# Kernel optimization log

Hardware: AMD Instinct MI355X
Metric: run time of the kernel (lower is better)

## Reference

```python
import jax, jax.numpy as jnp
import numpy as np
from jax import lax

B, S, T = 512, 64, 32
E, H = 512, 1024
VIN, VOUT = 128, 128


def gru_cell(x, h, W_ih, W_hh, b_ih, b_hh):
    # PyTorch GRU cell: gates ordered (r, z, n)
    gi = x @ W_ih.T + b_ih           # [B, 3*Hh]
    gh = h @ W_hh.T + b_hh           # [B, 3*Hh]
    i_r, i_z, i_n = jnp.split(gi, 3, axis=-1)
    h_r, h_z, h_n = jnp.split(gh, 3, axis=-1)
    r = jax.nn.sigmoid(i_r + h_r)
    z = jax.nn.sigmoid(i_z + h_z)
    n = jnp.tanh(i_n + r * h_n)
    return (1.0 - z) * n + z * h


def setup_inputs() -> dict:
    key = jax.random.key(0)
    ks = jax.random.split(key, 18)
    g = lambda k, shp: (jax.random.normal(k, shp, jnp.float32) * 0.05)
    return {
        "src": jax.random.randint(ks[0], (B, S), 0, VIN),
        "tgt": jax.random.randint(ks[1], (B, T), 0, VOUT),
        "enc_emb": g(ks[2], (VIN, E)),
        "dec_emb": g(ks[3], (VOUT, E)),
        "W_ih_f": g(ks[4], (3 * H, E)), "W_hh_f": g(ks[5], (3 * H, H)),
        "b_ih_f": g(ks[6], (3 * H,)), "b_hh_f": g(ks[7], (3 * H,)),
        "W_ih_b": g(ks[8], (3 * H, E)), "W_hh_b": g(ks[9], (3 * H, H)),
        "b_ih_b": g(ks[10], (3 * H,)), "b_hh_b": g(ks[11], (3 * H,)),
        "W_ih_d": g(ks[12], (3 * 2 * H, E)), "W_hh_d": g(ks[13], (3 * 2 * H, 2 * H)),
        "b_ih_d": g(ks[14], (3 * 2 * H,)), "b_hh_d": g(ks[15], (3 * 2 * H,)),
        "W_fc": g(ks[16], (VOUT, 2 * H)), "b_fc": g(ks[17], (VOUT,)),
    }


def reference(src, tgt, enc_emb, dec_emb,
              W_ih_f, W_hh_f, b_ih_f, b_hh_f,
              W_ih_b, W_hh_b, b_ih_b, b_hh_b,
              W_ih_d, W_hh_d, b_ih_d, b_hh_d,
              W_fc, b_fc):
    batch = src.shape[0]
    x = enc_emb[src]                         # [B, S, E]
    x_t = jnp.swapaxes(x, 0, 1)              # [S, B, E]

    def enc_scan(xs, W_ih, W_hh, b_ih, b_hh):
        h0 = jnp.zeros((batch, H), dtype=xs.dtype)
        def step(h, xt):
            h2 = gru_cell(xt, h, W_ih, W_hh, b_ih, b_hh)
            return h2, None
        hT, _ = lax.scan(step, h0, xs)
        return hT                             # final hidden [B, H]

    h_fwd = enc_scan(x_t, W_ih_f, W_hh_f, b_ih_f, b_hh_f)
    h_bwd = enc_scan(x_t[::-1], W_ih_b, W_hh_b, b_ih_b, b_hh_b)
    h = jnp.concatenate([h_fwd, h_bwd], axis=-1)   # [B, 2H] = torch.cat((h[-2], h[-1]), 1)

    tok0 = tgt[:, 0]                          # <sos> tokens

    def dec_step(carry, _):
        hh, tok = carry
        xt = dec_emb[tok]                     # [B, E]
        hh = gru_cell(xt, hh, W_ih_d, W_hh_d, b_ih_d, b_hh_d)
        logits = hh @ W_fc.T + b_fc           # [B, VOUT]
        nxt = jnp.argmax(logits, axis=-1)     # greedy feedback (teacher_forcing_ratio=0)
        return (hh, nxt), logits

    (_, _), logits = lax.scan(dec_step, (h, tok0), None, length=tgt.shape[1] - 1)
    return jnp.swapaxes(logits, 0, 1)         # [B, T-1, VOUT]
```

## Files before the change

### kernel.cpp

```cpp
#include <hip/hip_runtime.h>
#include <math.h>

#define B 512
#define S 64
#define T 32
#define E 512
#define H 1024
#define VOUTD 128
#define H2 (2*H)
#define H3 (3*H)
#define H6 (6*H)

#define LDR 40

typedef unsigned short ushortT;
typedef unsigned int uintT;
typedef __attribute__((ext_vector_type(8))) short short8;
typedef __attribute__((ext_vector_type(4))) float floatx4;

__device__ __forceinline__ float sigmoidf_(float x) { return 1.0f / (1.0f + expf(-x)); }

__global__ __launch_bounds__(256) void split_bf16(
    const float4* __restrict__ x, uint2* __restrict__ hi, uint2* __restrict__ lo, int n4)
{
    int i = blockIdx.x * 256 + threadIdx.x;
    if (i >= n4) return;
    float4 v = x[i];
    uintT ux = __float_as_uint(v.x), uy = __float_as_uint(v.y);
    uintT uz = __float_as_uint(v.z), uw = __float_as_uint(v.w);
    uintT lx = __float_as_uint(v.x - __uint_as_float(ux & 0xFFFF0000u)) >> 16;
    uintT ly = __float_as_uint(v.y - __uint_as_float(uy & 0xFFFF0000u)) >> 16;
    uintT lz = __float_as_uint(v.z - __uint_as_float(uz & 0xFFFF0000u)) >> 16;
    uintT lw = __float_as_uint(v.w - __uint_as_float(uw & 0xFFFF0000u)) >> 16;
    hi[i] = make_uint2((ux >> 16) | (uy & 0xFFFF0000u), (uz >> 16) | (uw & 0xFFFF0000u));
    lo[i] = make_uint2(lx | (ly << 16), lz | (lw << 16));
}

__global__ __launch_bounds__(256) void zero16(uint4* __restrict__ p, int n)
{
    int i = blockIdx.x * 256 + threadIdx.x;
    if (i < n) p[i] = make_uint4(0u, 0u, 0u, 0u);
}

__global__ __launch_bounds__(256) void fused_step_enc(
    const ushortT* __restrict__ Ahi, const ushortT* __restrict__ Alo,
    const ushortT* __restrict__ Whi_f, const ushortT* __restrict__ Wlo_f,
    const ushortT* __restrict__ Whi_b, const ushortT* __restrict__ Wlo_b,
    const float* __restrict__ giTabF, const float* __restrict__ giTabB,
    const int* __restrict__ src, int s,
    const float* __restrict__ bhF, const float* __restrict__ bhB,
    float* __restrict__ h,
    ushortT* __restrict__ hiOut, ushortT* __restrict__ loOut)
{
    __shared__ ushortT sAh[2][64 * LDR], sAl[2][64 * LDR];
    __shared__ ushortT sBh[2][96 * LDR], sBl[2][96 * LDR];
    __shared__ int sTok[64];

    const int t    = threadIdx.x;
    const int lane = t & 63;
    const int w    = t >> 6;

    const int bid = blockIdx.x;
    const int xcd = bid & 7;
    const int q   = bid >> 3;
    const int jg  = xcd + 8 * (q & 3);
    const int mb  = q >> 2;
    const int j0  = jg * 32;
    const int m0  = mb * 64;
    const bool bwd = (m0 >= B);

    const ushortT* Whi   = bwd ? Whi_b : Whi_f;
    const ushortT* Wlo   = bwd ? Wlo_b : Wlo_f;
    const float*   giTab = bwd ? giTabB : giTabF;
    const float*   bh    = bwd ? bhB : bhF;

    if (t < 64) {
        int b = (m0 + t) & (B - 1);
        sTok[t] = src[b * S + (bwd ? (S - 1 - s) : s)];
    }

    const int kseg = (t & 3) * 8;
    const ushortT* gAh = Ahi + (size_t)(m0 + (t >> 2)) * H + kseg;
    const ushortT* gAl = Alo + (size_t)(m0 + (t >> 2)) * H + kseg;
    const int brow0 = t >> 2;
    const int wr0   = (brow0 >> 5) * H + j0 + (brow0 & 31);
    const ushortT* gBh0 = Whi + (size_t)wr0 * H + kseg;
    const ushortT* gBl0 = Wlo + (size_t)wr0 * H + kseg;
    const int brow1 = 64 + (t >> 2);
    const int wr1   = (brow1 >> 5) * H + j0 + (brow1 & 31);
    const ushortT* gBh1 = Whi + (size_t)wr1 * H + kseg;
    const ushortT* gBl1 = Wlo + (size_t)wr1 * H + kseg;
    const int ldsA  = (t >> 2) * LDR + kseg;
    const int ldsB0 = (t >> 2) * LDR + kseg;
    const int ldsB1 = (64 + (t >> 2)) * LDR + kseg;
    const bool doB1 = (t < 128);

    const int koff = (lane >> 4) * 8;
    const int rA0  = (w >> 1) * 32 + (lane & 15);
    const int rB0  = (w & 1) * 16 + (lane & 15);

    floatx4 acc[2][3];
#pragma unroll
    for (int mi = 0; mi < 2; ++mi)
#pragma unroll
        for (int g = 0; g < 3; ++g) acc[mi][g] = (floatx4){0.f, 0.f, 0.f, 0.f};

    uint4 vAh, vAl, vBh0, vBl0, vBh1 = {}, vBl1 = {};
    vAh  = *(const uint4*)gAh;  vAl  = *(const uint4*)gAl;
    vBh0 = *(const uint4*)gBh0; vBl0 = *(const uint4*)gBl0;
    if (doB1) { vBh1 = *(const uint4*)gBh1; vBl1 = *(const uint4*)gBl1; }
    *(uint4*)&sAh[0][ldsA]  = vAh;  *(uint4*)&sAl[0][ldsA]  = vAl;
    *(uint4*)&sBh[0][ldsB0] = vBh0; *(uint4*)&sBl[0][ldsB0] = vBl0;
    if (doB1) { *(uint4*)&sBh[0][ldsB1] = vBh1; *(uint4*)&sBl[0][ldsB1] = vBl1; }
    __syncthreads();

    int p = 0;
    const int nCh = H / 32;
    for (int ck = 0; ck < nCh; ++ck) {
        const bool hasNext = (ck + 1 < nCh);
        if (hasNext) {
            const int k0 = (ck + 1) * 32;
            vAh  = *(const uint4*)(gAh + k0);  vAl  = *(const uint4*)(gAl + k0);
            vBh0 = *(const uint4*)(gBh0 + k0); vBl0 = *(const uint4*)(gBl0 + k0);
            if (doB1) { vBh1 = *(const uint4*)(gBh1 + k0); vBl1 = *(const uint4*)(gBl1 + k0); }
        }
        short8 fah[2], fal[2], fbh[3], fbl[3];
#pragma unroll
        for (int mi = 0; mi < 2; ++mi) {
            fah[mi] = *(const short8*)&sAh[p][(rA0 + mi * 16) * LDR + koff];
            fal[mi] = *(const short8*)&sAl[p][(rA0 + mi * 16) * LDR + koff];
        }
#pragma unroll
        for (int g = 0; g < 3; ++g) {
            fbh[g] = *(const short8*)&sBh[p][(rB0 + g * 32) * LDR + koff];
            fbl[g] = *(const short8*)&sBl[p][(rB0 + g * 32) * LDR + koff];
        }
#pragma unroll
        for (int mi = 0; mi < 2; ++mi)
#pragma unroll
            for (int g = 0; g < 3; ++g) {
                acc[mi][g] = __builtin_amdgcn_mfma_f32_16x16x32_bf16(fah[mi], fbh[g], acc[mi][g], 0, 0, 0);
                acc[mi][g] = __builtin_amdgcn_mfma_f32_16x16x32_bf16(fah[mi], fbl[g], acc[mi][g], 0, 0, 0);
                acc[mi][g] = __builtin_amdgcn_mfma_f32_16x16x32_bf16(fal[mi], fbh[g], acc[mi][g], 0, 0, 0);
            }
        if (hasNext) {
            const int pq = p ^ 1;
            *(uint4*)&sAh[pq][ldsA]  = vAh;  *(uint4*)&sAl[pq][ldsA]  = vAl;
            *(uint4*)&sBh[pq][ldsB0] = vBh0; *(uint4*)&sBl[pq][ldsB0] = vBl0;
            if (doB1) { *(uint4*)&sBh[pq][ldsB1] = vBh1; *(uint4*)&sBl[pq][ldsB1] = vBl1; }
            __syncthreads();
            p = pq;
        }
    }

    const int colj = j0 + (w & 1) * 16 + (lane & 15);
    const float bR = bh[colj], bZ = bh[H + colj], bN = bh[2 * H + colj];
    const int rloc0 = (w >> 1) * 32 + (lane >> 4) * 4;
#pragma unroll
    for (int mi = 0; mi < 2; ++mi) {
#pragma unroll
        for (int r = 0; r < 4; ++r) {
            const int rloc = rloc0 + mi * 16 + r;
            const int row  = m0 + rloc;
            const float* gi = giTab + (size_t)sTok[rloc] * H3;
            float ghr = acc[mi][0][r] + bR;
            float ghz = acc[mi][1][r] + bZ;
            float ghn = acc[mi][2][r] + bN;
            float rr = sigmoidf_(gi[colj] + ghr);
            float z  = sigmoidf_(gi[H + colj] + ghz);
            float n  = tanhf(gi[2 * H + colj] + rr * ghn);
            const size_t idx = (size_t)row * H + colj;
            float hnew = (1.0f - z) * n + z * h[idx];
            h[idx] = hnew;
            uintT u = __float_as_uint(hnew);
            hiOut[idx] = (ushortT)(u >> 16);
            loOut[idx] = (ushortT)(__float_as_uint(hnew - __uint_as_float(u & 0xFFFF0000u)) >> 16);
        }
    }
}

__global__ __launch_bounds__(256) void fused_step_dec(
    const ushortT* __restrict__ Ahi, const ushortT* __restrict__ Alo,
    const ushortT* __restrict__ Whi, const ushortT* __restrict__ Wlo,
    const float* __restrict__ giTabD, const int* __restrict__ tok,
    const float* __restrict__ bhD,
    float* __restrict__ h,
    ushortT* __restrict__ hiOut, ushortT* __restrict__ loOut)
{
    __shared__ ushortT sAh[2][64 * LDR], sAl[2][64 * LDR];
    __shared__ ushortT sBh[2][96 * LDR], sBl[2][96 * LDR];
    __shared__ int sTok[64];

    const int t    = threadIdx.x;
    const int lane = t & 63;
    const int w    = t >> 6;

    const int bid = blockIdx.x;
    const int xcd = bid & 7;
    const int q   = bid >> 3;
    const int jg  = xcd + 8 * (q & 7);
    const int mb  = q >> 3;
    const int j0  = jg * 32;
    const int m0  = mb * 64;

    if (t < 64) sTok[t] = tok[m0 + t];

    const int kseg = (t & 3) * 8;
    const ushortT* gAh = Ahi + (size_t)(m0 + (t >> 2)) * H2 + kseg;
    const ushortT* gAl = Alo + (size_t)(m0 + (t >> 2)) * H2 + kseg;
    const int brow0 = t >> 2;
    const int wr0   = (brow0 >> 5) * H2 + j0 + (brow0 & 31);
    const ushortT* gBh0 = Whi + (size_t)wr0 * H2 + kseg;
    const ushortT* gBl0 = Wlo + (size_t)wr0 * H2 + kseg;
    const int brow1 = 64 + (t >> 2);
    const int wr1   = (brow1 >> 5) * H2 + j0 + (brow1 & 31);
    const ushortT* gBh1 = Whi + (size_t)wr1 * H2 + kseg;
    const ushortT* gBl1 = Wlo + (size_t)wr1 * H2 + kseg;
    const int ldsA  = (t >> 2) * LDR + kseg;
    const int ldsB0 = (t >> 2) * LDR + kseg;
    const int ldsB1 = (64 + (t >> 2)) * LDR + kseg;
    const bool doB1 = (t < 128);

    const int koff = (lane >> 4) * 8;
    const int rA0  = (w >> 1) * 32 + (lane & 15);
    const int rB0  = (w & 1) * 16 + (lane & 15);

    floatx4 acc[2][3];
#pragma unroll
    for (int mi = 0; mi < 2; ++mi)
#pragma unroll
        for (int g = 0; g < 3; ++g) acc[mi][g] = (floatx4){0.f, 0.f, 0.f, 0.f};

    uint4 vAh, vAl, vBh0, vBl0, vBh1 = {}, vBl1 = {};
    vAh  = *(const uint4*)gAh;  vAl  = *(const uint4*)gAl;
    vBh0 = *(const uint4*)gBh0; vBl0 = *(const uint4*)gBl0;
    if (doB1) { vBh1 = *(const uint4*)gBh1; vBl1 = *(const uint4*)gBl1; }
    *(uint4*)&sAh[0][ldsA]  = vAh;  *(uint4*)&sAl[0][ldsA]  = vAl;
    *(uint4*)&sBh[0][ldsB0] = vBh0; *(uint4*)&sBl[0][ldsB0] = vBl0;
    if (doB1) { *(uint4*)&sBh[0][ldsB1] = vBh1; *(uint4*)&sBl[0][ldsB1] = vBl1; }
    __syncthreads();

    int p = 0;
    const int nCh = H2 / 32;
    for (int ck = 0; ck < nCh; ++ck) {
        const bool hasNext = (ck + 1 < nCh);
        if (hasNext) {
            const int k0 = (ck + 1) * 32;
            vAh  = *(const uint4*)(gAh + k0);  vAl  = *(const uint4*)(gAl + k0);
            vBh0 = *(const uint4*)(gBh0 + k0); vBl0 = *(const uint4*)(gBl0 + k0);
            if (doB1) { vBh1 = *(const uint4*)(gBh1 + k0); vBl1 = *(const uint4*)(gBl1 + k0); }
        }
        short8 fah[2], fal[2], fbh[3], fbl[3];
#pragma unroll
        for (int mi = 0; mi < 2; ++mi) {
            fah[mi] = *(const short8*)&sAh[p][(rA0 + mi * 16) * LDR + koff];
            fal[mi] = *(const short8*)&sAl[p][(rA0 + mi * 16) * LDR + koff];
        }
#pragma unroll
        for (int g = 0; g < 3; ++g) {
            fbh[g] = *(const short8*)&sBh[p][(rB0 + g * 32) * LDR + koff];
            fbl[g] = *(const short8*)&sBl[p][(rB0 + g * 32) * LDR + koff];
        }
#pragma unroll
        for (int mi = 0; mi < 2; ++mi)
#pragma unroll
            for (int g = 0; g < 3; ++g) {
                acc[mi][g] = __builtin_amdgcn_mfma_f32_16x16x32_bf16(fah[mi], fbh[g], acc[mi][g], 0, 0, 0);
                acc[mi][g] = __builtin_amdgcn_mfma_f32_16x16x32_bf16(fah[mi], fbl[g], acc[mi][g], 0, 0, 0);
                acc[mi][g] = __builtin_amdgcn_mfma_f32_16x16x32_bf16(fal[mi], fbh[g], acc[mi][g], 0, 0, 0);
            }
        if (hasNext) {
            const int pq = p ^ 1;
            *(uint4*)&sAh[pq][ldsA]  = vAh;  *(uint4*)&sAl[pq][ldsA]  = vAl;
            *(uint4*)&sBh[pq][ldsB0] = vBh0; *(uint4*)&sBl[pq][ldsB0] = vBl0;
            if (doB1) { *(uint4*)&sBh[pq][ldsB1] = vBh1; *(uint4*)&sBl[pq][ldsB1] = vBl1; }
            __syncthreads();
            p = pq;
        }
    }

    const int colj = j0 + (w & 1) * 16 + (lane & 15);
    const float bR = bhD[colj], bZ = bhD[H2 + colj], bN = bhD[2 * H2 + colj];
    const int rloc0 = (w >> 1) * 32 + (lane >> 4) * 4;
#pragma unroll
    for (int mi = 0; mi < 2; ++mi) {
#pragma unroll
        for (int r = 0; r < 4; ++r) {
            const int rloc = rloc0 + mi * 16 + r;
            const int row  = m0 + rloc;
            const float* gi = giTabD + (size_t)sTok[rloc] * H6;
            float ghr = acc[mi][0][r] + bR;
            float ghz = acc[mi][1][r] + bZ;
            float ghn = acc[mi][2][r] + bN;
            float rr = sigmoidf_(gi[colj] + ghr);
            float z  = sigmoidf_(gi[H2 + colj] + ghz);
            float n  = tanhf(gi[2 * H2 + colj] + rr * ghn);
            const size_t idx = (size_t)row * H2 + colj;
            float hnew = (1.0f - z) * n + z * h[idx];
            h[idx] = hnew;
            uintT u = __float_as_uint(hnew);
            hiOut[idx] = (ushortT)(u >> 16);
            loOut[idx] = (ushortT)(__float_as_uint(hnew - __uint_as_float(u & 0xFFFF0000u)) >> 16);
        }
    }
}

__global__ __launch_bounds__(256) void init_hh_tok_split(
    const float* __restrict__ h_f, const float* __restrict__ h_b,
    const int* __restrict__ tgt, float* __restrict__ hh,
    ushortT* __restrict__ hh_hi, ushortT* __restrict__ hh_lo, int* __restrict__ tok)
{
    int i = blockIdx.x * blockDim.x + threadIdx.x;
    int b = i >> 11;
    int j = i & 2047;
    float v = (j < H) ? h_f[(size_t)b * H + j] : h_b[(size_t)b * H + (j - H)];
    hh[i] = v;
    uintT u = __float_as_uint(v);
    hh_hi[i] = (ushortT)(u >> 16);
    hh_lo[i] = (ushortT)(__float_as_uint(v - __uint_as_float(u & 0xFFFF0000u)) >> 16);
    if (j == 0) tok[b] = tgt[b * T];
}

__global__ __launch_bounds__(256) void logits_argmax2(
    const float* __restrict__ hh, const float* __restrict__ W_fc,
    const float* __restrict__ b_fc, float* __restrict__ out,
    int* __restrict__ tok, int t)
{
    __shared__ float sh[2][H2];
    __shared__ float sred[2][2][128];
    __shared__ float sval[2][128];
    __shared__ int   sidx[2][128];
    const int tid = threadIdx.x;
    const int col = tid & 127;
    const int kh  = tid >> 7;
    const int b0  = blockIdx.x * 2;

    {
        const float4* srcp = (const float4*)(hh + (size_t)b0 * H2);
        float4* dst = (float4*)sh;
        for (int i = tid; i < 2 * H2 / 4; i += 256) dst[i] = srcp[i];
    }
    __syncthreads();

    const float* wrow = W_fc + (size_t)col * H2 + kh * (H2 / 2);
    const float* s0 = sh[0] + kh * (H2 / 2);
    const float* s1 = sh[1] + kh * (H2 / 2);
    float a0 = 0.f, a1 = 0.f;
#pragma unroll 8
    for (int k = 0; k < H2 / 2; k += 4) {
        float4 w4 = *(const float4*)(wrow + k);
        float4 h0 = *(const float4*)(s0 + k);
        float4 h1 = *(const float4*)(s1 + k);
        a0 += w4.x * h0.x + w4.y * h0.y + w4.z * h0.z + w4.w * h0.w;
        a1 += w4.x * h1.x + w4.y * h1.y + w4.z * h1.z + w4.w * h1.w;
    }
    sred[kh][0][col] = a0;
    sred[kh][1][col] = a1;
    __syncthreads();

    if (kh == 0) {
        float l0 = sred[0][0][col] + sred[1][0][col] + b_fc[col];
        float l1 = sred[0][1][col] + sred[1][1][col] + b_fc[col];
        out[(size_t)(b0 + 0) * ((T - 1) * VOUTD) + (size_t)t * VOUTD + col] = l0;
        out[(size_t)(b0 + 1) * ((T - 1) * VOUTD) + (size_t)t * VOUTD + col] = l1;
        sval[0][col] = l0; sidx[0][col] = col;
        sval[1][col] = l1; sidx[1][col] = col;
    }
    __syncthreads();

    const int r = tid >> 7, c = tid & 127;
    for (int off = 64; off > 0; off >>= 1) {
        if (c < off) {
// ... 108 lines not shown
__global__ __launch_bounds__(256) void gru_gate(
    const float* __restrict__ gi, const float* __restrict__ gh,
    float* __restrict__ h, int Hd)
{
    int i = blockIdx.x * blockDim.x + threadIdx.x;
    int b = i / Hd, j = i - b * Hd;
    const float* gib = gi + (size_t)b * 3 * Hd;
    const float* ghb = gh + (size_t)b * 3 * Hd;
    float r = sigmoidf_(gib[j] + ghb[j]);
    float z = sigmoidf_(gib[Hd + j] + ghb[Hd + j]);
    float n = tanhf(gib[2 * Hd + j] + r * ghb[2 * Hd + j]);
    h[i] = (1.0f - z) * n + z * h[i];
}

__global__ __launch_bounds__(256) void init_hh_tok(
    const float* __restrict__ h_f, const float* __restrict__ h_b,
    const int* __restrict__ tgt, float* __restrict__ hh, int* __restrict__ tok)
{
    int i = blockIdx.x * blockDim.x + threadIdx.x;
    int b = i >> 11, j = i & 2047;
    hh[i] = (j < H) ? h_f[(size_t)b * H + j] : h_b[(size_t)b * H + (j - H)];
    if (j == 0) tok[b] = tgt[b * T];
}

extern "C" void kernel_launch(void* const* d_in, const int* in_sizes, int n_in,
                              void* d_out, int out_size, void* d_ws, size_t ws_size,
                              hipStream_t stream)
{
    const int*   src     = (const int*)d_in[0];
    const int*   tgt     = (const int*)d_in[1];
    const float* enc_emb = (const float*)d_in[2];
    const float* dec_emb = (const float*)d_in[3];
    const float* W_ih_f  = (const float*)d_in[4];
    const float* W_hh_f  = (const float*)d_in[5];
    const float* b_ih_f  = (const float*)d_in[6];
    const float* b_hh_f  = (const float*)d_in[7];
    const float* W_ih_b  = (const float*)d_in[8];
    const float* W_hh_b  = (const float*)d_in[9];
    const float* b_ih_b  = (const float*)d_in[10];
    const float* b_hh_b  = (const float*)d_in[11];
    const float* W_ih_d  = (const float*)d_in[12];
    const float* W_hh_d  = (const float*)d_in[13];
    const float* b_ih_d  = (const float*)d_in[14];
    const float* b_hh_d  = (const float*)d_in[15];
    const float* W_fc    = (const float*)d_in[16];
    const float* b_fc    = (const float*)d_in[17];
    float* out = (float*)d_out;

    char* base = (char*)d_ws;
    size_t off = 0;
    auto alloc = [&](size_t bytes) { char* p = base + off; off += (bytes + 255) & ~(size_t)255; return p; };

    float*   hE     = (float*)  alloc((size_t)2 * B * H * 4);
    ushortT* hE_hi  = (ushortT*)alloc((size_t)2 * B * H * 2);
    ushortT* hE_lo  = (ushortT*)alloc((size_t)2 * B * H * 2);
    float*   hh     = (float*)  alloc((size_t)B * H2 * 4);
    ushortT* hh_hi  = (ushortT*)alloc((size_t)B * H2 * 2);
    ushortT* hh_lo  = (ushortT*)alloc((size_t)B * H2 * 2);
    float*   ghE    = (float*)  alloc((size_t)2 * 2 * B * H3 * 4);
    float*   giTabF = (float*)  alloc((size_t)VOUTD * H3 * 4);
    float*   giTabB = (float*)  alloc((size_t)VOUTD * H3 * 4);
    float*   giTabD = (float*)  alloc((size_t)VOUTD * H6 * 4);
    ushortT* Whhf_hi = (ushortT*)alloc((size_t)H3 * H * 2);
    ushortT* Whhf_lo = (ushortT*)alloc((size_t)H3 * H * 2);
    ushortT* Whhb_hi = (ushortT*)alloc((size_t)H3 * H * 2);
    ushortT* Whhb_lo = (ushortT*)alloc((size_t)H3 * H * 2);
    ushortT* Whhd_hi = (ushortT*)alloc((size_t)H6 * H2 * 2);
    ushortT* Whhd_lo = (ushortT*)alloc((size_t)H6 * H2 * 2);
    int*     tok    = (int*)    alloc((size_t)B * 4);
    float*   giE    = ghE;
    size_t required = off;

    char* ghBase = (char*)ghE;
    ushortT* hE_hiB = (ushortT*)(ghBase);
    ushortT* hE_loB = (ushortT*)(ghBase + (size_t)2 * B * H * 2);
    ushortT* hh_hiB = (ushortT*)(ghBase + (size_t)4 * B * H * 2);
    ushortT* hh_loB = (ushortT*)(ghBase + (size_t)4 * B * H * 2 + (size_t)B * H2 * 2);

    dim3 blk(256);

    if (ws_size >= required) {
        {
            size_t zbytes = (size_t)2 * B * H * 4 + 2 * ((size_t)2 * B * H * 2);
            int n16 = (int)(zbytes / 16);
            zero16<<<dim3((n16 + 255) / 256), blk, 0, stream>>>((uint4*)hE, n16);
        }
        auto split = [&](const float* x, ushortT* hi, ushortT* lo, size_t n) {
            int n4 = (int)(n / 4);
            split_bf16<<<dim3((n4 + 255) / 256), blk, 0, stream>>>(
                (const float4*)x, (uint2*)hi, (uint2*)lo, n4);
        };
        split(W_hh_f, Whhf_hi, Whhf_lo, (size_t)H3 * H);
        split(W_hh_b, Whhb_hi, Whhb_lo, (size_t)H3 * H);
        split(W_hh_d, Whhd_hi, Whhd_lo, (size_t)H6 * H2);

        gemm_bias<<<dim3(H3 / 64, VOUTD / 64), blk, 0, stream>>>(
            enc_emb, nullptr, 0, 0, E, W_ih_f, b_ih_f, giTabF, H3, E);
        gemm_bias<<<dim3(H3 / 64, VOUTD / 64), blk, 0, stream>>>(
            enc_emb, nullptr, 0, 0, E, W_ih_b, b_ih_b, giTabB, H3, E);
        gemm_bias<<<dim3(H6 / 64, VOUTD / 64), blk, 0, stream>>>(
            dec_emb, nullptr, 0, 0, E, W_ih_d, b_ih_d, giTabD, H6, E);

        for (int s = 0; s < S; ++s) {
            const ushortT* inHi = (s & 1) ? hE_hiB : hE_hi;
            const ushortT* inLo = (s & 1) ? hE_loB : hE_lo;
            ushortT* outHi = (s & 1) ? hE_hi : hE_hiB;
            ushortT* outLo = (s & 1) ? hE_lo : hE_loB;
            fused_step_enc<<<dim3(512), blk, 0, stream>>>(
                inHi, inLo, Whhf_hi, Whhf_lo, Whhb_hi, Whhb_lo,
                giTabF, giTabB, src, s, b_hh_f, b_hh_b,
                hE, outHi, outLo);
        }

        init_hh_tok_split<<<dim3((B * H2) / 256), blk, 0, stream>>>(
            hE, hE + (size_t)B * H, tgt, hh, hh_hi, hh_lo, tok);

        for (int t = 0; t < T - 1; ++t) {
            const ushortT* inHi = (t & 1) ? hh_hiB : hh_hi;
            const ushortT* inLo = (t & 1) ? hh_loB : hh_lo;
            ushortT* outHi = (t & 1) ? hh_hi : hh_hiB;
            ushortT* outLo = (t & 1) ? hh_lo : hh_loB;
            fused_step_dec<<<dim3(512), blk, 0, stream>>>(
                inHi, inLo, Whhd_hi, Whhd_lo, giTabD, tok, b_hh_d,
                hh, outHi, outLo);
            logits_argmax2<<<dim3(B / 2), blk, 0, stream>>>(hh, W_fc, b_fc, out, tok, t);
        }
    } else {
        {
            size_t zbytes = (size_t)2 * B * H * 4;
            int n16 = (int)(zbytes / 16);
            zero16<<<dim3((n16 + 255) / 256), blk, 0, stream>>>((uint4*)hE, n16);
        }
        float* ghF = giE + (size_t)2 * B * H3;
        dim3 grid_gi(H3 / 64, (2 * B) / 64);
        dim3 grid_gate((2 * B * H) / 256);
        for (int s = 0; s < S; ++s) {
            gemm_enc<<<grid_gi, blk, 0, stream>>>(enc_emb, E, E, src, s,
                                                  W_ih_f, b_ih_f, W_ih_b, b_ih_b, giE, H3);
            gemm_enc<<<grid_gi, blk, 0, stream>>>(hE, H, H, nullptr, 0,
                                                  W_hh_f, b_hh_f, W_hh_b, b_hh_b, ghF, H3);
            gru_gate<<<grid_gate, blk, 0, stream>>>(giE, ghF, hE, H);
        }
        init_hh_tok<<<dim3((B * H2) / 256), blk, 0, stream>>>(hE, hE + (size_t)B * H, tgt, hh, tok);
        dim3 grid_d(H6 / 64, B / 64);
        dim3 grid_dgate((B * H2) / 256);
        for (int t = 0; t < T - 1; ++t) {
            gemm_bias<<<grid_d, blk, 0, stream>>>(dec_emb, tok, 1, 0, E,
                                                  W_ih_d, b_ih_d, giE, H6, E);
            gemm_bias<<<grid_d, blk, 0, stream>>>(hh, nullptr, 0, 0, H2,
                                                  W_hh_d, b_hh_d, ghF, H6, H2);
            gru_gate<<<grid_dgate, blk, 0, stream>>>(giE, ghF, hh, H2);
            logits_argmax2<<<dim3(B / 2), blk, 0, stream>>>(hh, W_fc, b_fc, out, tok, t);
        }
    }
}
```

Measured before the change: 5.248 ms.

## Store weights and hidden state pre-swizzled in MFMA fragment layout

Weights are converted once into a bf16 hi/lo layout that matches the MFMA 16x16x32 fragment order. The hidden state is written directly in fragment order, so A operands are loaded straight from global memory into registers with no LDS staging. B tiles are still double-buffered through LDS but are now copied contiguously, with no padded rows, and two K-chunks are handled per iteration. The intent is fewer LDS bytes, fewer barriers, and coalesced fragment loads, at the cost of scattered 2-byte stores in the epilogue and a more complex indexing scheme.

```diff
diff --git a/kernel.cpp b/kernel.cpp
--- a/kernel.cpp
+++ b/kernel.cpp
@@ -11,8 +11,6 @@
 #define H3 (3*H)
 #define H6 (6*H)
 
-#define LDR 40
-
 typedef unsigned short ushortT;
 typedef unsigned int uintT;
 typedef __attribute__((ext_vector_type(8))) short short8;
@@ -20,20 +18,14 @@
 
 __device__ __forceinline__ float sigmoidf_(float x) { return 1.0f / (1.0f + expf(-x)); }
 
-__global__ __launch_bounds__(256) void split_bf16(
-    const float4* __restrict__ x, uint2* __restrict__ hi, uint2* __restrict__ lo, int n4)
-{
-    int i = blockIdx.x * 256 + threadIdx.x;
-    if (i >= n4) return;
-    float4 v = x[i];
-    uintT ux = __float_as_uint(v.x), uy = __float_as_uint(v.y);
-    uintT uz = __float_as_uint(v.z), uw = __float_as_uint(v.w);
-    uintT lx = __float_as_uint(v.x - __uint_as_float(ux & 0xFFFF0000u)) >> 16;
-    uintT ly = __float_as_uint(v.y - __uint_as_float(uy & 0xFFFF0000u)) >> 16;
-    uintT lz = __float_as_uint(v.z - __uint_as_float(uz & 0xFFFF0000u)) >> 16;
-    uintT lw = __float_as_uint(v.w - __uint_as_float(uw & 0xFFFF0000u)) >> 16;
-    hi[i] = make_uint2((ux >> 16) | (uy & 0xFFFF0000u), (uz >> 16) | (uw & 0xFFFF0000u));
-    lo[i] = make_uint2(lx | (ly << 16), lz | (lw << 16));
+__device__ __forceinline__ uintT pack_hi2(float a, float b) {
+    return (__float_as_uint(a) >> 16) | (__float_as_uint(b) & 0xFFFF0000u);
+}
+__device__ __forceinline__ uintT pack_lo2(float a, float b) {
+    uintT ua = __float_as_uint(a), ub = __float_as_uint(b);
+    uintT la = __float_as_uint(a - __uint_as_float(ua & 0xFFFF0000u)) >> 16;
+    uintT lb = __float_as_uint(b - __uint_as_float(ub & 0xFFFF0000u)) >> 16;
+    return la | (lb << 16);
 }
 
 __global__ __launch_bounds__(256) void zero16(uint4* __restrict__ p, int n)
@@ -42,62 +34,75 @@
     if (i < n) p[i] = make_uint4(0u, 0u, 0u, 0u);
 }
 
+__global__ __launch_bounds__(256) void swizzle_w(
+    const float* __restrict__ W, ushortT* __restrict__ out, int njShift, int kShift)
+{
+    int idx = blockIdx.x * 256 + threadIdx.x;
+    int total = 3 << (njShift + kShift);
+    if (idx >= total) return;
+    int wrow = idx >> kShift;
+    int k8 = idx & ((1 << kShift) - 1);
+    int k = k8 << 3;
+    int K = 8 << kShift;
+    const float* s = W + (size_t)wrow * K + k;
+    float4 f0 = *(const float4*)s;
+    float4 f1 = *(const float4*)(s + 4);
+    int g = wrow >> njShift;
+    int j = wrow & ((1 << njShift) - 1);
+    int jb = j >> 4, jl = j & 15;
+    int c = k >> 5, kq = (k >> 3) & 3;
+    int laneA = jl + 16 * kq;
+    int ncK = K >> 5;
+    size_t base = (((size_t)(jb * ncK + c) * 3 + g) * 2) * 512 + (size_t)laneA * 8;
+    uint4 hv = make_uint4(pack_hi2(f0.x, f0.y), pack_hi2(f0.z, f0.w),
+                          pack_hi2(f1.x, f1.y), pack_hi2(f1.z, f1.w));
+    uint4 lv = make_uint4(pack_lo2(f0.x, f0.y), pack_lo2(f0.z, f0.w),
+                          pack_lo2(f1.x, f1.y), pack_lo2(f1.z, f1.w));
+    *(uint4*)(out + base) = hv;
+    *(uint4*)(out + base + 512) = lv;
+}
+
 __global__ __launch_bounds__(256) void fused_step_enc(
-    const ushortT* __restrict__ Ahi, const ushortT* __restrict__ Alo,
-    const ushortT* __restrict__ Whi_f, const ushortT* __restrict__ Wlo_f,
-    const ushortT* __restrict__ Whi_b, const ushortT* __restrict__ Wlo_b,
+    const ushortT* __restrict__ Afr,
+    const ushortT* __restrict__ WfrF, const ushortT* __restrict__ WfrB,
     const float* __restrict__ giTabF, const float* __restrict__ giTabB,
     const int* __restrict__ src, int s,
     const float* __restrict__ bhF, const float* __restrict__ bhB,
-    float* __restrict__ h,
-    ushortT* __restrict__ hiOut, ushortT* __restrict__ loOut)
-{
-    __shared__ ushortT sAh[2][64 * LDR], sAl[2][64 * LDR];
-    __shared__ ushortT sBh[2][96 * LDR], sBl[2][96 * LDR];
+    float* __restrict__ h, ushortT* __restrict__ AfrOut)
+{
+    __shared__ ushortT sB[2][24 * 512];
     __shared__ int sTok[64];
-
-    const int t    = threadIdx.x;
-    const int lane = t & 63;
-    const int w    = t >> 6;
-
+    const int t = threadIdx.x, lane = t & 63, w = t >> 6;
     const int bid = blockIdx.x;
-    const int xcd = bid & 7;
-    const int q   = bid >> 3;
-    const int jg  = xcd + 8 * (q & 3);
-    const int mb  = q >> 2;
-    const int j0  = jg * 32;
-    const int m0  = mb * 64;
+    const int xcd = bid & 7, q = bid >> 3;
+    const int jg = xcd + 8 * (q & 3);
+    const int mb = q >> 2;
+    const int j0 = jg * 32, m0 = mb * 64;
     const bool bwd = (m0 >= B);
-
-    const ushortT* Whi   = bwd ? Whi_b : Whi_f;
-    const ushortT* Wlo   = bwd ? Wlo_b : Wlo_f;
-    const float*   giTab = bwd ? giTabB : giTabF;
-    const float*   bh    = bwd ? bhB : bhF;
+    const ushortT* Wfr = bwd ? WfrB : WfrF;
+    const float* giTab = bwd ? giTabB : giTabF;
+    const float* bh = bwd ? bhB : bhF;
+    const int NCK = 32, NIT = 16;
 
     if (t < 64) {
         int b = (m0 + t) & (B - 1);
         sTok[t] = src[b * S + (bwd ? (S - 1 - s) : s)];
     }
 
-    const int kseg = (t & 3) * 8;
-    const ushortT* gAh = Ahi + (size_t)(m0 + (t >> 2)) * H + kseg;
-    const ushortT* gAl = Alo + (size_t)(m0 + (t >> 2)) * H + kseg;
-    const int brow0 = t >> 2;
-    const int wr0   = (brow0 >> 5) * H + j0 + (brow0 & 31);
-    const ushortT* gBh0 = Whi + (size_t)wr0 * H + kseg;
-    const ushortT* gBl0 = Wlo + (size_t)wr0 * H + kseg;
-    const int brow1 = 64 + (t >> 2);
-    const int wr1   = (brow1 >> 5) * H + j0 + (brow1 & 31);
-    const ushortT* gBh1 = Whi + (size_t)wr1 * H + kseg;
-    const ushortT* gBl1 = Wlo + (size_t)wr1 * H + kseg;
-    const int ldsA  = (t >> 2) * LDR + kseg;
-    const int ldsB0 = (t >> 2) * LDR + kseg;
-    const int ldsB1 = (64 + (t >> 2)) * LDR + kseg;
-    const bool doB1 = (t < 128);
-
-    const int koff = (lane >> 4) * 8;
-    const int rA0  = (w >> 1) * 32 + (lane & 15);
-    const int rB0  = (w & 1) * 16 + (lane & 15);
+    const int wr = w >> 1, wc = w & 1;
+    const ushortT* aP = Afr + (size_t)((m0 >> 4) + wr * 2) * (NCK * 1024) + lane * 8;
+
+    const ushortT* gWb[3];
+    int lds0[3], lds1[3];
+#pragma unroll
+    for (int k = 0; k < 3; ++k) {
+        int f = w * 3 + k;
+        int jbLoc = f / 6, rem = f % 6;
+        gWb[k] = Wfr + (size_t)(jg * 2 + jbLoc) * (NCK * 3072) + rem * 512 + lane * 8;
+        lds0[k] = f * 512 + lane * 8;
+        lds1[k] = (12 + f) * 512 + lane * 8;
+    }
+    const int rb0 = wc * 3072 + lane * 8;
 
     floatx4 acc[2][3];
 #pragma unroll
@@ -105,63 +110,96 @@
 #pragma unroll
         for (int g = 0; g < 3; ++g) acc[mi][g] = (floatx4){0.f, 0.f, 0.f, 0.f};
 
-    uint4 vAh, vAl, vBh0, vBl0, vBh1 = {}, vBl1 = {};
-    vAh  = *(const uint4*)gAh;  vAl  = *(const uint4*)gAl;
-    vBh0 = *(const uint4*)gBh0; vBl0 = *(const uint4*)gBl0;
-    if (doB1) { vBh1 = *(const uint4*)gBh1; vBl1 = *(const uint4*)gBl1; }
-    *(uint4*)&sAh[0][ldsA]  = vAh;  *(uint4*)&sAl[0][ldsA]  = vAl;
-    *(uint4*)&sBh[0][ldsB0] = vBh0; *(uint4*)&sBl[0][ldsB0] = vBl0;
-    if (doB1) { *(uint4*)&sBh[0][ldsB1] = vBh1; *(uint4*)&sBl[0][ldsB1] = vBl1; }
+    uint4 st0[3], st1[3];
+#pragma unroll
+    for (int k = 0; k < 3; ++k) {
+        st0[k] = *(const uint4*)(gWb[k]);
+        st1[k] = *(const uint4*)(gWb[k] + 3072);
+    }
+#pragma unroll
+    for (int k = 0; k < 3; ++k) {
+        *(uint4*)&sB[0][lds0[k]] = st0[k];
+        *(uint4*)&sB[0][lds1[k]] = st1[k];
+    }
     __syncthreads();
 
-    int p = 0;
-    const int nCh = H / 32;
-    for (int ck = 0; ck < nCh; ++ck) {
-        const bool hasNext = (ck + 1 < nCh);
-        if (hasNext) {
-            const int k0 = (ck + 1) * 32;
-            vAh  = *(const uint4*)(gAh + k0);  vAl  = *(const uint4*)(gAl + k0);
-            vBh0 = *(const uint4*)(gBh0 + k0); vBl0 = *(const uint4*)(gBl0 + k0);
-            if (doB1) { vBh1 = *(const uint4*)(gBh1 + k0); vBl1 = *(const uint4*)(gBl1 + k0); }
-        }
-        short8 fah[2], fal[2], fbh[3], fbl[3];
-#pragma unroll
-        for (int mi = 0; mi < 2; ++mi) {
-            fah[mi] = *(const short8*)&sAh[p][(rA0 + mi * 16) * LDR + koff];
-            fal[mi] = *(const short8*)&sAl[p][(rA0 + mi * 16) * LDR + koff];
-        }
-#pragma unroll
-        for (int g = 0; g < 3; ++g) {
-            fbh[g] = *(const short8*)&sBh[p][(rB0 + g * 32) * LDR + koff];
-            fbl[g] = *(const short8*)&sBl[p][(rB0 + g * 32) * LDR + koff];
-        }
-#pragma unroll
-        for (int mi = 0; mi < 2; ++mi)
+    short8 an00 = *(const short8*)(aP);
+    short8 an01 = *(const short8*)(aP + 512);
+    short8 an10 = *(const short8*)(aP + NCK * 1024);
+    short8 an11 = *(const short8*)(aP + NCK * 1024 + 512);
+
+    int pb = 0;
+    for (int it = 0; it < NIT; ++it) {
+        if (it + 1 < NIT) {
+            int cb = (it + 1) * 2;
+#pragma unroll
+            for (int k = 0; k < 3; ++k) {
+                st0[k] = *(const uint4*)(gWb[k] + (size_t)cb * 3072);
+                st1[k] = *(const uint4*)(gWb[k] + (size_t)(cb + 1) * 3072);
+            }
+        }
+        const ushortT* bp = &sB[pb][0];
+        {
+            short8 a00 = an00, a01 = an01, a10 = an10, a11 = an11;
+            int cn = 2 * it + 1;
+            an00 = *(const short8*)(aP + (size_t)cn * 1024);
+            an01 = *(const short8*)(aP + (size_t)cn * 1024 + 512);
+            an10 = *(const short8*)(aP + (size_t)cn * 1024 + NCK * 1024);
+            an11 = *(const short8*)(aP + (size_t)cn * 1024 + NCK * 1024 + 512);
 #pragma unroll
             for (int g = 0; g < 3; ++g) {
-                acc[mi][g] = __builtin_amdgcn_mfma_f32_16x16x32_bf16(fah[mi], fbh[g], acc[mi][g], 0, 0, 0);
-                acc[mi][g] = __builtin_amdgcn_mfma_f32_16x16x32_bf16(fah[mi], fbl[g], acc[mi][g], 0, 0, 0);
-                acc[mi][g] = __builtin_amdgcn_mfma_f32_16x16x32_bf16(fal[mi], fbh[g], acc[mi][g], 0, 0, 0);
-            }
-        if (hasNext) {
-            const int pq = p ^ 1;
-            *(uint4*)&sAh[pq][ldsA]  = vAh;  *(uint4*)&sAl[pq][ldsA]  = vAl;
-            *(uint4*)&sBh[pq][ldsB0] = vBh0; *(uint4*)&sBl[pq][ldsB0] = vBl0;
-            if (doB1) { *(uint4*)&sBh[pq][ldsB1] = vBh1; *(uint4*)&sBl[pq][ldsB1] = vBl1; }
+                short8 bhf = *(const short8*)&bp[rb0 + g * 1024];
+                short8 blf = *(const short8*)&bp[rb0 + g * 1024 + 512];
+                acc[0][g] = __builtin_amdgcn_mfma_f32_16x16x32_bf16(a00, bhf, acc[0][g], 0, 0, 0);
+                acc[0][g] = __builtin_amdgcn_mfma_f32_16x16x32_bf16(a00, blf, acc[0][g], 0, 0, 0);
+                acc[0][g] = __builtin_amdgcn_mfma_f32_16x16x32_bf16(a01, bhf, acc[0][g], 0, 0, 0);
+                acc[1][g] = __builtin_amdgcn_mfma_f32_16x16x32_bf16(a10, bhf, acc[1][g], 0, 0, 0);
+                acc[1][g] = __builtin_amdgcn_mfma_f32_16x16x32_bf16(a10, blf, acc[1][g], 0, 0, 0);
+                acc[1][g] = __builtin_amdgcn_mfma_f32_16x16x32_bf16(a11, bhf, acc[1][g], 0, 0, 0);
+            }
+        }
+        {
+            short8 a00 = an00, a01 = an01, a10 = an10, a11 = an11;
+            int cn = 2 * it + 2; if (cn >= NCK) cn = NCK - 1;
+            an00 = *(const short8*)(aP + (size_t)cn * 1024);
+            an01 = *(const short8*)(aP + (size_t)cn * 1024 + 512);
+            an10 = *(const short8*)(aP + (size_t)cn * 1024 + NCK * 1024);
+            an11 = *(const short8*)(aP + (size_t)cn * 1024 + NCK * 1024 + 512);
+#pragma unroll
+            for (int g = 0; g < 3; ++g) {
+                short8 bhf = *(const short8*)&bp[12 * 512 + rb0 + g * 1024];
+                short8 blf = *(const short8*)&bp[12 * 512 + rb0 + g * 1024 + 512];
+                acc[0][g] = __builtin_amdgcn_mfma_f32_16x16x32_bf16(a00, bhf, acc[0][g], 0, 0, 0);
+                acc[0][g] = __builtin_amdgcn_mfma_f32_16x16x32_bf16(a00, blf, acc[0][g], 0, 0, 0);
+                acc[0][g] = __builtin_amdgcn_mfma_f32_16x16x32_bf16(a01, bhf, acc[0][g], 0, 0, 0);
+                acc[1][g] = __builtin_amdgcn_mfma_f32_16x16x32_bf16(a10, bhf, acc[1][g], 0, 0, 0);
+                acc[1][g] = __builtin_amdgcn_mfma_f32_16x16x32_bf16(a10, blf, acc[1][g], 0, 0, 0);
+                acc[1][g] = __builtin_amdgcn_mfma_f32_16x16x32_bf16(a11, bhf, acc[1][g], 0, 0, 0);
+            }
+        }
+        if (it + 1 < NIT) {
+#pragma unroll
+            for (int k = 0; k < 3; ++k) {
+                *(uint4*)&sB[pb ^ 1][lds0[k]] = st0[k];
+                *(uint4*)&sB[pb ^ 1][lds1[k]] = st1[k];
+            }
             __syncthreads();
-            p = pq;
-        }
-    }
-
-    const int colj = j0 + (w & 1) * 16 + (lane & 15);
+            pb ^= 1;
+        }
+    }
+
+    const int colj = j0 + wc * 16 + (lane & 15);
     const float bR = bh[colj], bZ = bh[H + colj], bN = bh[2 * H + colj];
-    const int rloc0 = (w >> 1) * 32 + (lane >> 4) * 4;
+    const int rloc0 = wr * 32 + (lane >> 4) * 4;
+    const int cA = colj >> 5;
+    const int kqA = (colj >> 3) & 3;
+    const int eA = colj & 7;
 #pragma unroll
     for (int mi = 0; mi < 2; ++mi) {
 #pragma unroll
         for (int r = 0; r < 4; ++r) {
             const int rloc = rloc0 + mi * 16 + r;
-            const int row  = m0 + rloc;
+            const int row = m0 + rloc;
             const float* gi = giTab + (size_t)sTok[rloc] * H3;
             float ghr = acc[mi][0][r] + bR;
             float ghz = acc[mi][1][r] + bZ;
@@ -173,57 +211,46 @@
             float hnew = (1.0f - z) * n + z * h[idx];
             h[idx] = hnew;
             uintT u = __float_as_uint(hnew);
-            hiOut[idx] = (ushortT)(u >> 16);
-            loOut[idx] = (ushortT)(__float_as_uint(hnew - __uint_as_float(u & 0xFFFF0000u)) >> 16);
+            size_t ao = (((size_t)(row >> 4) * 32 + cA) * 2) * 512
+                      + (size_t)((row & 15) + 16 * kqA) * 8 + eA;
+            AfrOut[ao] = (ushortT)(u >> 16);
+            AfrOut[ao + 512] = (ushortT)(__float_as_uint(hnew - __uint_as_float(u & 0xFFFF0000u)) >> 16);
         }
     }
 }
 
 __global__ __launch_bounds__(256) void fused_step_dec(
-    const ushortT* __restrict__ Ahi, const ushortT* __restrict__ Alo,
-    const ushortT* __restrict__ Whi, const ushortT* __restrict__ Wlo,
+    const ushortT* __restrict__ Afr, const ushortT* __restrict__ Wfr,
     const float* __restrict__ giTabD, const int* __restrict__ tok,
     const float* __restrict__ bhD,
-    float* __restrict__ h,
-    ushortT* __restrict__ hiOut, ushortT* __restrict__ loOut)
-{
-    __shared__ ushortT sAh[2][64 * LDR], sAl[2][64 * LDR];
-    __shared__ ushortT sBh[2][96 * LDR], sBl[2][96 * LDR];
+    float* __restrict__ h, ushortT* __restrict__ AfrOut)
+{
+    __shared__ ushortT sB[2][24 * 512];
     __shared__ int sTok[64];
-
-    const int t    = threadIdx.x;
-    const int lane = t & 63;
-    const int w    = t >> 6;
-
+    const int t = threadIdx.x, lane = t & 63, w = t >> 6;
     const int bid = blockIdx.x;
-    const int xcd = bid & 7;
-    const int q   = bid >> 3;
-    const int jg  = xcd + 8 * (q & 7);
-    const int mb  = q >> 3;
-    const int j0  = jg * 32;
-    const int m0  = mb * 64;
+    const int xcd = bid & 7, q = bid >> 3;
+    const int jg = xcd + 8 * (q & 7);
+    const int mb = q >> 3;
+    const int j0 = jg * 32, m0 = mb * 64;
+    const int NCK = 64, NIT = 32;
 
     if (t < 64) sTok[t] = tok[m0 + t];
 
-    const int kseg = (t & 3) * 8;
-    const ushortT* gAh = Ahi + (size_t)(m0 + (t >> 2)) * H2 + kseg;
-    const ushortT* gAl = Alo + (size_t)(m0 + (t >> 2)) * H2 + kseg;
-    const int brow0 = t >> 2;
-    const int wr0   = (brow0 >> 5) * H2 + j0 + (brow0 & 31);
-    const ushortT* gBh0 = Whi + (size_t)wr0 * H2 + kseg;
-    const ushortT* gBl0 = Wlo + (size_t)wr0 * H2 + kseg;
-    const int brow1 = 64 + (t >> 2);
-    const int wr1   = (brow1 >> 5) * H2 + j0 + (brow1 & 31);
-    const ushortT* gBh1 = Whi + (size_t)wr1 * H2 + kseg;
-    const ushortT* gBl1 = Wlo + (size_t)wr1 * H2 + kseg;
-    const int ldsA  = (t >> 2) * LDR + kseg;
-    const int ldsB0 = (t >> 2) * LDR + kseg;
-    const int ldsB1 = (64 + (t >> 2)) * LDR + kseg;
-    const bool doB1 = (t < 128);
-
-    const int koff = (lane >> 4) * 8;
-    const int rA0  = (w >> 1) * 32 + (lane & 15);
-    const int rB0  = (w & 1) * 16 + (lane & 15);
+    const int wr = w >> 1, wc = w & 1;
+    const ushortT* aP = Afr + (size_t)((m0 >> 4) + wr * 2) * (NCK * 1024) + lane * 8;
+
+    const ushortT* gWb[3];
+    int lds0[3], lds1[3];
+#pragma unroll
+    for (int k = 0; k < 3; ++k) {
+        int f = w * 3 + k;
+        int jbLoc = f / 6, rem = f % 6;
+        gWb[k] = Wfr + (size_t)(jg * 2 + jbLoc) * (NCK * 3072) + rem * 512 + lane * 8;
+        lds0[k] = f * 512 + lane * 8;
+        lds1[k] = (12 + f) * 512 + lane * 8;
+    }
+    const int rb0 = wc * 3072 + lane * 8;
 
     floatx4 acc[2][3];
 #pragma unroll
@@ -231,63 +258,96 @@
 #pragma unroll
         for (int g = 0; g < 3; ++g) acc[mi][g] = (floatx4){0.f, 0.f, 0.f, 0.f};
 
-    uint4 vAh, vAl, vBh0, vBl0, vBh1 = {}, vBl1 = {};
-    vAh  = *(const uint4*)gAh;  vAl  = *(const uint4*)gAl;
-    vBh0 = *(const uint4*)gBh0; vBl0 = *(const uint4*)gBl0;
-    if (doB1) { vBh1 = *(const uint4*)gBh1; vBl1 = *(const uint4*)gBl1; }
-    *(uint4*)&sAh[0][ldsA]  = vAh;  *(uint4*)&sAl[0][ldsA]  = vAl;
-    *(uint4*)&sBh[0][ldsB0] = vBh0; *(uint4*)&sBl[0][ldsB0] = vBl0;
-    if (doB1) { *(uint4*)&sBh[0][ldsB1] = vBh1; *(uint4*)&sBl[0][ldsB1] = vBl1; }
+    uint4 st0[3], st1[3];
+#pragma unroll
+    for (int k = 0; k < 3; ++k) {
+        st0[k] = *(const uint4*)(gWb[k]);
+        st1[k] = *(const uint4*)(gWb[k] + 3072);
+    }
+#pragma unroll
+    for (int k = 0; k < 3; ++k) {
+        *(uint4*)&sB[0][lds0[k]] = st0[k];
+        *(uint4*)&sB[0][lds1[k]] = st1[k];
+    }
     __syncthreads();
 
-    int p = 0;
-    const int nCh = H2 / 32;
-    for (int ck = 0; ck < nCh; ++ck) {
-        const bool hasNext = (ck + 1 < nCh);
-        if (hasNext) {
-            const int k0 = (ck + 1) * 32;
-            vAh  = *(const uint4*)(gAh + k0);  vAl  = *(const uint4*)(gAl + k0);
-            vBh0 = *(const uint4*)(gBh0 + k0); vBl0 = *(const uint4*)(gBl0 + k0);
-            if (doB1) { vBh1 = *(const uint4*)(gBh1 + k0); vBl1 = *(const uint4*)(gBl1 + k0); }
-        }
-        short8 fah[2], fal[2], fbh[3], fbl[3];
-#pragma unroll
-        for (int mi = 0; mi < 2; ++mi) {
-            fah[mi] = *(const short8*)&sAh[p][(rA0 + mi * 16) * LDR + koff];
-            fal[mi] = *(const short8*)&sAl[p][(rA0 + mi * 16) * LDR + koff];
-        }
-#pragma unroll
-        for (int g = 0; g < 3; ++g) {
-            fbh[g] = *(const short8*)&sBh[p][(rB0 + g * 32) * LDR + koff];
-            fbl[g] = *(const short8*)&sBl[p][(rB0 + g * 32) * LDR + koff];
-        }
-#pragma unroll
-        for (int mi = 0; mi < 2; ++mi)
+    short8 an00 = *(const short8*)(aP);
+    short8 an01 = *(const short8*)(aP + 512);
+    short8 an10 = *(const short8*)(aP + NCK * 1024);
+    short8 an11 = *(const short8*)(aP + NCK * 1024 + 512);
+
+    int pb = 0;
+    for (int it = 0; it < NIT; ++it) {
+        if (it + 1 < NIT) {
+            int cb = (it + 1) * 2;
+#pragma unroll
+            for (int k = 0; k < 3; ++k) {
+                st0[k] = *(const uint4*)(gWb[k] + (size_t)cb * 3072);
+                st1[k] = *(const uint4*)(gWb[k] + (size_t)(cb + 1) * 3072);
+            }
+        }
+        const ushortT* bp = &sB[pb][0];
+        {
+            short8 a00 = an00, a01 = an01, a10 = an10, a11 = an11;
+            int cn = 2 * it + 1;
+            an00 = *(const short8*)(aP + (size_t)cn * 1024);
+            an01 = *(const short8*)(aP + (size_t)cn * 1024 + 512);
+            an10 = *(const short8*)(aP + (size_t)cn * 1024 + NCK * 1024);
+            an11 = *(const short8*)(aP + (size_t)cn * 1024 + NCK * 1024 + 512);
 #pragma unroll
             for (int g = 0; g < 3; ++g) {
-                acc[mi][g] = __builtin_amdgcn_mfma_f32_16x16x32_bf16(fah[mi], fbh[g], acc[mi][g], 0, 0, 0);
-                acc[mi][g] = __builtin_amdgcn_mfma_f32_16x16x32_bf16(fah[mi], fbl[g], acc[mi][g], 0, 0, 0);
-                acc[mi][g] = __builtin_amdgcn_mfma_f32_16x16x32_bf16(fal[mi], fbh[g], acc[mi][g], 0, 0, 0);
-            }
-        if (hasNext) {
-            const int pq = p ^ 1;
-            *(uint4*)&sAh[pq][ldsA]  = vAh;  *(uint4*)&sAl[pq][ldsA]  = vAl;
-            *(uint4*)&sBh[pq][ldsB0] = vBh0; *(uint4*)&sBl[pq][ldsB0] = vBl0;
-            if (doB1) { *(uint4*)&sBh[pq][ldsB1] = vBh1; *(uint4*)&sBl[pq][ldsB1] = vBl1; }
+                short8 bhf = *(const short8*)&bp[rb0 + g * 1024];
+                short8 blf = *(const short8*)&bp[rb0 + g * 1024 + 512];
+                acc[0][g] = __builtin_amdgcn_mfma_f32_16x16x32_bf16(a00, bhf, acc[0][g], 0, 0, 0);
+                acc[0][g] = __builtin_amdgcn_mfma_f32_16x16x32_bf16(a00, blf, acc[0][g], 0, 0, 0);
+                acc[0][g] = __builtin_amdgcn_mfma_f32_16x16x32_bf16(a01, bhf, acc[0][g], 0, 0, 0);
+                acc[1][g] = __builtin_amdgcn_mfma_f32_16x16x32_bf16(a10, bhf, acc[1][g], 0, 0, 0);
+                acc[1][g] = __builtin_amdgcn_mfma_f32_16x16x32_bf16(a10, blf, acc[1][g], 0, 0, 0);
+                acc[1][g] = __builtin_amdgcn_mfma_f32_16x16x32_bf16(a11, bhf, acc[1][g], 0, 0, 0);
+            }
+        }
+        {
+            short8 a00 = an00, a01 = an01, a10 = an10, a11 = an11;
+            int cn = 2 * it + 2; if (cn >= NCK) cn = NCK - 1;
+            an00 = *(const short8*)(aP + (size_t)cn * 1024);
+            an01 = *(const short8*)(aP + (size_t)cn * 1024 + 512);
+            an10 = *(const short8*)(aP + (size_t)cn * 1024 + NCK * 1024);
+            an11 = *(const short8*)(aP + (size_t)cn * 1024 + NCK * 1024 + 512);
+#pragma unroll
+            for (int g = 0; g < 3; ++g) {
+                short8 bhf = *(const short8*)&bp[12 * 512 + rb0 + g * 1024];
+                short8 blf = *(const short8*)&bp[12 * 512 + rb0 + g * 1024 + 512];
+                acc[0][g] = __builtin_amdgcn_mfma_f32_16x16x32_bf16(a00, bhf, acc[0][g], 0, 0, 0);
+                acc[0][g] = __builtin_amdgcn_mfma_f32_16x16x32_bf16(a00, blf, acc[0][g], 0, 0, 0);
+                acc[0][g] = __builtin_amdgcn_mfma_f32_16x16x32_bf16(a01, bhf, acc[0][g], 0, 0, 0);
+                acc[1][g] = __builtin_amdgcn_mfma_f32_16x16x32_bf16(a10, bhf, acc[1][g], 0, 0, 0);
+                acc[1][g] = __builtin_amdgcn_mfma_f32_16x16x32_bf16(a10, blf, acc[1][g], 0, 0, 0);
+                acc[1][g] = __builtin_amdgcn_mfma_f32_16x16x32_bf16(a11, bhf, acc[1][g], 0, 0, 0);
+            }
+        }
+        if (it + 1 < NIT) {
+#pragma unroll
+            for (int k = 0; k < 3; ++k) {
+                *(uint4*)&sB[pb ^ 1][lds0[k]] = st0[k];
+                *(uint4*)&sB[pb ^ 1][lds1[k]] = st1[k];
+            }
             __syncthreads();
-            p = pq;
-        }
-    }
-
-    const int colj = j0 + (w & 1) * 16 + (lane & 15);
+            pb ^= 1;
+        }
+    }
+
+    const int colj = j0 + wc * 16 + (lane & 15);
     const float bR = bhD[colj], bZ = bhD[H2 + colj], bN = bhD[2 * H2 + colj];
-    const int rloc0 = (w >> 1) * 32 + (lane >> 4) * 4;
+    const int rloc0 = wr * 32 + (lane >> 4) * 4;
+    const int cA = colj >> 5;
+    const int kqA = (colj >> 3) & 3;
+    const int eA = colj & 7;
 #pragma unroll
     for (int mi = 0; mi < 2; ++mi) {
 #pragma unroll
         for (int r = 0; r < 4; ++r) {
             const int rloc = rloc0 + mi * 16 + r;
-            const int row  = m0 + rloc;
+            const int row = m0 + rloc;
             const float* gi = giTabD + (size_t)sTok[rloc] * H6;
             float ghr = acc[mi][0][r] + bR;
             float ghz = acc[mi][1][r] + bZ;
@@ -299,8 +359,10 @@
             float hnew = (1.0f - z) * n + z * h[idx];
             h[idx] = hnew;
             uintT u = __float_as_uint(hnew);
-            hiOut[idx] = (ushortT)(u >> 16);
-            loOut[idx] = (ushortT)(__float_as_uint(hnew - __uint_as_float(u & 0xFFFF0000u)) >> 16);
+            size_t ao = (((size_t)(row >> 4) * 64 + cA) * 2) * 512
+                      + (size_t)((row & 15) + 16 * kqA) * 8 + eA;
+            AfrOut[ao] = (ushortT)(u >> 16);
+            AfrOut[ao + 512] = (ushortT)(__float_as_uint(hnew - __uint_as_float(u & 0xFFFF0000u)) >> 16);
         }
     }
 }
@@ -308,7 +370,7 @@
 __global__ __launch_bounds__(256) void init_hh_tok_split(
     const float* __restrict__ h_f, const float* __restrict__ h_b,
     const int* __restrict__ tgt, float* __restrict__ hh,
-    ushortT* __restrict__ hh_hi, ushortT* __restrict__ hh_lo, int* __restrict__ tok)
+    ushortT* __restrict__ AfrD, int* __restrict__ tok)
 {
     int i = blockIdx.x * blockDim.x + threadIdx.x;
     int b = i >> 11;
@@ -316,8 +378,10 @@
     float v = (j < H) ? h_f[(size_t)b * H + j] : h_b[(size_t)b * H + (j - H)];
     hh[i] = v;
     uintT u = __float_as_uint(v);
-    hh_hi[i] = (ushortT)(u >> 16);
-    hh_lo[i] = (ushortT)(__float_as_uint(v - __uint_as_float(u & 0xFFFF0000u)) >> 16);
+    size_t ao = (((size_t)(b >> 4) * 64 + (j >> 5)) * 2) * 512
+              + (size_t)((b & 15) + 16 * ((j >> 3) & 3)) * 8 + (j & 7);
+    AfrD[ao] = (ushortT)(u >> 16);
+    AfrD[ao + 512] = (ushortT)(__float_as_uint(v - __uint_as_float(u & 0xFFFF0000u)) >> 16);
     if (j == 0) tok[b] = tgt[b * T];
 }
 
@@ -532,47 +596,32 @@
     auto alloc = [&](size_t bytes) { char* p = base + off; off += (bytes + 255) & ~(size_t)255; return p; };
 
     float*   hE     = (float*)  alloc((size_t)2 * B * H * 4);
-    ushortT* hE_hi  = (ushortT*)alloc((size_t)2 * B * H * 2);
-    ushortT* hE_lo  = (ushortT*)alloc((size_t)2 * B * H * 2);
+    ushortT* AfrEA  = (ushortT*)alloc((size_t)2 * B * H * 2 * 2);
+    ushortT* AfrEB  = (ushortT*)alloc((size_t)2 * B * H * 2 * 2);
     float*   hh     = (float*)  alloc((size_t)B * H2 * 4);
-    ushortT* hh_hi  = (ushortT*)alloc((size_t)B * H2 * 2);
-    ushortT* hh_lo  = (ushortT*)alloc((size_t)B * H2 * 2);
-    float*   ghE    = (float*)  alloc((size_t)2 * 2 * B * H3 * 4);
+    ushortT* AfrDA  = (ushortT*)alloc((size_t)B * H2 * 2 * 2);
+    ushortT* AfrDB  = (ushortT*)alloc((size_t)B * H2 * 2 * 2);
     float*   giTabF = (float*)  alloc((size_t)VOUTD * H3 * 4);
     float*   giTabB = (float*)  alloc((size_t)VOUTD * H3 * 4);
     float*   giTabD = (float*)  alloc((size_t)VOUTD * H6 * 4);
-    ushortT* Whhf_hi = (ushortT*)alloc((size_t)H3 * H * 2);
-    ushortT* Whhf_lo = (ushortT*)alloc((size_t)H3 * H * 2);
-    ushortT* Whhb_hi = (ushortT*)alloc((size_t)H3 * H * 2);
-    ushortT* Whhb_lo = (ushortT*)alloc((size_t)H3 * H * 2);
-    ushortT* Whhd_hi = (ushortT*)alloc((size_t)H6 * H2 * 2);
-    ushortT* Whhd_lo = (ushortT*)alloc((size_t)H6 * H2 * 2);
+    ushortT* WfrF   = (ushortT*)alloc((size_t)H3 * H * 2 * 2);
+    ushortT* WfrB   = (ushortT*)alloc((size_t)H3 * H * 2 * 2);
+    ushortT* WfrD   = (ushortT*)alloc((size_t)H6 * H2 * 2 * 2);
     int*     tok    = (int*)    alloc((size_t)B * 4);
-    float*   giE    = ghE;
     size_t required = off;
-
-    char* ghBase = (char*)ghE;
-    ushortT* hE_hiB = (ushortT*)(ghBase);
-    ushortT* hE_loB = (ushortT*)(ghBase + (size_t)2 * B * H * 2);
-    ushortT* hh_hiB = (ushortT*)(ghBase + (size_t)4 * B * H * 2);
-    ushortT* hh_loB = (ushortT*)(ghBase + (size_t)4 * B * H * 2 + (size_t)B * H2 * 2);
 
     dim3 blk(256);
 
     if (ws_size >= required) {
         {
-            size_t zbytes = (size_t)2 * B * H * 4 + 2 * ((size_t)2 * B * H * 2);
+            size_t zbytes = (size_t)2 * B * H * 4 + (size_t)2 * B * H * 4;
             int n16 = (int)(zbytes / 16);
             zero16<<<dim3((n16 + 255) / 256), blk, 0, stream>>>((uint4*)hE, n16);
         }
-        auto split = [&](const float* x, ushortT* hi, ushortT* lo, size_t n) {
-            int n4 = (int)(n / 4);
-            split_bf16<<<dim3((n4 + 255) / 256), blk, 0, stream>>>(
-                (const float4*)x, (uint2*)hi, (uint2*)lo, n4);
-        };
-        split(W_hh_f, Whhf_hi, Whhf_lo, (size_t)H3 * H);
-        split(W_hh_b, Whhb_hi, Whhb_lo, (size_t)H3 * H);
-        split(W_hh_d, Whhd_hi, Whhd_lo, (size_t)H6 * H2);
+        swizzle_w<<<dim3((3 * H3 * H / (3 * 8) * 3 / 256) ? ((3 << 17) + 255) / 256 : 1), blk, 0, stream>>>(
+            W_hh_f, WfrF, 10, 7);
+        swizzle_w<<<dim3(((3 << 17) + 255) / 256), blk, 0, stream>>>(W_hh_b, WfrB, 10, 7);
+        swizzle_w<<<dim3(((3 << 19) + 255) / 256), blk, 0, stream>>>(W_hh_d, WfrD, 11, 8);
 
         gemm_bias<<<dim3(H3 / 64, VOUTD / 64), blk, 0, stream>>>(
             enc_emb, nullptr, 0, 0, E, W_ih_f, b_ih_f, giTabF, H3, E);
@@ -582,27 +631,20 @@
             dec_emb, nullptr, 0, 0, E, W_ih_d, b_ih_d, giTabD, H6, E);
 
         for (int s = 0; s < S; ++s) {
-            const ushortT* inHi = (s & 1) ? hE_hiB : hE_hi;
-            const ushortT* inLo = (s & 1) ? hE_loB : hE_lo;
-            ushortT* outHi = (s & 1) ? hE_hi : hE_hiB;
-            ushortT* outLo = (s & 1) ? hE_lo : hE_loB;
+            const ushortT* inA = (s & 1) ? AfrEB : AfrEA;
+            ushortT* outA = (s & 1) ? AfrEA : AfrEB;
             fused_step_enc<<<dim3(512), blk, 0, stream>>>(
-                inHi, inLo, Whhf_hi, Whhf_lo, Whhb_hi, Whhb_lo,
-                giTabF, giTabB, src, s, b_hh_f, b_hh_b,
-                hE, outHi, outLo);
+                inA, WfrF, WfrB, giTabF, giTabB, src, s, b_hh_f, b_hh_b, hE, outA);
         }
 
         init_hh_tok_split<<<dim3((B * H2) / 256), blk, 0, stream>>>(
-            hE, hE + (size_t)B * H, tgt, hh, hh_hi, hh_lo, tok);
+            hE, hE + (size_t)B * H, tgt, hh, AfrDA, tok);
 
         for (int t = 0; t < T - 1; ++t) {
-            const ushortT* inHi = (t & 1) ? hh_hiB : hh_hi;
-            const ushortT* inLo = (t & 1) ? hh_loB : hh_lo;
-            ushortT* outHi = (t & 1) ? hh_hi : hh_hiB;
-            ushortT* outLo = (t & 1) ? hh_lo : hh_loB;
+            const ushortT* inA = (t & 1) ? AfrDB : AfrDA;
+            ushortT* outA = (t & 1) ? AfrDA : AfrDB;
             fused_step_dec<<<dim3(512), blk, 0, stream>>>(
-                inHi, inLo, Whhd_hi, Whhd_lo, giTabD, tok, b_hh_d,
-                hh, outHi, outLo);
+                inA, WfrD, giTabD, tok, b_hh_d, hh, outA);
             logits_argmax2<<<dim3(B / 2), blk, 0, stream>>>(hh, W_fc, b_fc, out, tok, t);
         }
     } else {
@@ -611,6 +653,7 @@
             int n16 = (int)(zbytes / 16);
             zero16<<<dim3((n16 + 255) / 256), blk, 0, stream>>>((uint4*)hE, n16);
         }
+        float* giE = (float*)WfrF;
         float* ghF = giE + (size_t)2 * B * H3;
         dim3 grid_gi(H3 / 64, (2 * B) / 64);
         dim3 grid_gate((2 * B * H) / 256);
```

Measured after the change: 4.854 ms. 1.08x faster.
